# Performance work log

Measured on AMD Instinct MI355X. Metric: run time of the kernel, lower is better.

Reference implementation:

```python
import jax, jax.numpy as jnp
import numpy as np

SEQ = 2048
HIDDEN = 2048
INPUT = 2048
THETA = 3
TRUNC = 128  # truncated-BPTT length (divides SEQ)


def setup_inputs() -> dict:
    key = jax.random.key(0)
    k0, k1, k2, k3, k4 = jax.random.split(key, 5)
    inp = jax.random.normal(k0, (1, SEQ, INPUT), jnp.float32)
    internal = jax.random.normal(k1, (THETA + 1, SEQ, HIDDEN), jnp.float32) * 0.1
    state = jax.random.normal(k2, (1, 1, HIDDEN), jnp.float32) * 0.1
    weight_ih = jax.random.normal(k3, (HIDDEN, INPUT), jnp.float32) / np.sqrt(INPUT).astype(np.float32)
    weight_hh = jax.random.normal(k4, (HIDDEN, HIDDEN), jnp.float32) * np.float32(0.5 / np.sqrt(HIDDEN))
    bias = jnp.zeros((HIDDEN,), jnp.float32)
    return {"input": inp, "internal": internal, "state": state,
            "weight_ih": weight_ih, "weight_hh": weight_hh, "bias": bias,
            "theta": THETA}


def reference(input, internal, state, weight_ih, weight_hh, bias, theta):
    theta = int(theta)
    seq = input.shape[1]
    hidden = weight_hh.shape[0]
    # pad input along theta dim to theta+1 (torch: F.pad with zeros at the end of dim 0)
    x = jnp.pad(input, ((0, theta + 1 - input.shape[0]), (0, 0), (0, 0)))
    # Precompute the input-driven part of the cell for every (theta, t):
    # cell: h' = relu(x @ Wih^T + internal + bias + h @ Whh^T)
    pre = jnp.einsum('tsi,hi->tsh', x, weight_ih) + internal + bias  # [theta+1, seq, hidden]
    n_chunks = seq // TRUNC
    # [n_chunks, TRUNC, theta+1, hidden]
    pre_c = pre.transpose(1, 0, 2).reshape(n_chunks, TRUNC, theta + 1, hidden)

    def cell(p, h):
        return jax.nn.relu(p + h @ weight_hh.T)

    def step(h, pre_t):  # pre_t: [theta+1, hidden]
        h0 = cell(pre_t[0], h)
        outs = [h0]
        hth = h0
        for th in range(1, theta + 1):
            hth = cell(pre_t[th], hth)
            outs.append(hth)
        # continuousTheta=False: carry state from the base (th=0) step
        return h0, jnp.stack(outs, 0)  # [theta+1, hidden]

    def chunk(h, pre_chunk):
        h, outs = jax.lax.scan(step, h, pre_chunk)
        # truncated BPTT: detach state between chunks (identity in fwd)
        return jax.lax.stop_gradient(h), outs

    h0 = state[0, 0]  # [hidden]
    h_final, outs = jax.lax.scan(chunk, h0, pre_c)
    # outs: [n_chunks, TRUNC, theta+1, hidden] -> [theta+1, seq, hidden]
    outputs = outs.reshape(seq, theta + 1, hidden).transpose(1, 0, 2)
    return outputs, h_final[None, None, :]
```

## Files before the change

### kernel.cpp

```cpp
#include <hip/hip_runtime.h>
#include <stdint.h>

#define SEQ 2048
#define HID 2048
#define INP 2048
#define NTH 4
#define K3  (HID*3)

typedef uint32_t u32x4  __attribute__((ext_vector_type(4)));
typedef short    short8 __attribute__((ext_vector_type(8)));
typedef float    f32x4  __attribute__((ext_vector_type(4)));
typedef uint32_t uint4v __attribute__((ext_vector_type(4)));

template<int CTRL>
__device__ __forceinline__ float dpp_add(float x) {
    int y = __builtin_amdgcn_update_dpp(0, __float_as_int(x), CTRL, 0xF, 0xF, true);
    return x + __int_as_float(y);
}
__device__ __forceinline__ float wave_sum64(float x) {
    x = dpp_add<0x111>(x); x = dpp_add<0x112>(x); x = dpp_add<0x114>(x);
    x = dpp_add<0x118>(x); x = dpp_add<0x142>(x); x = dpp_add<0x143>(x);
    return x;
}

__device__ __forceinline__ ushort bf16h(float x) {
    uint32_t u = __float_as_uint(x);
    return (ushort)((u + 0x7fffu + ((u >> 16) & 1u)) >> 16);
}
template<int BSIDE>
__global__ __launch_bounds__(256)
void convert3_k(const float* __restrict__ X, ushort* __restrict__ X3) {
    const size_t t = (size_t)blockIdx.x * 256 + threadIdx.x;
    float xs[8];
    *reinterpret_cast<float4*>(&xs[0]) = *reinterpret_cast<const float4*>(X + t * 8);
    *reinterpret_cast<float4*>(&xs[4]) = *reinterpret_cast<const float4*>(X + t * 8 + 4);
    ushort o[24];
#pragma unroll
    for (int i = 0; i < 8; ++i) {
        const ushort hi = bf16h(xs[i]);
        const float hif = __uint_as_float(((uint32_t)hi) << 16);
        const ushort lo = bf16h(xs[i] - hif);
        o[i * 3 + 0] = hi;
        o[i * 3 + 1] = BSIDE ? lo : hi;
        o[i * 3 + 2] = BSIDE ? hi : lo;
    }
    ushort* pd = X3 + t * 24;
#pragma unroll
    for (int v = 0; v < 3; ++v)
        *reinterpret_cast<uint4v*>(pd + v * 8) = *reinterpret_cast<const uint4v*>(&o[v * 8]);
}

template<int RELU>
__global__ __launch_bounds__(256, 2)
void mfma_gemm(const ushort* __restrict__ A3, const ushort* __restrict__ B3,
               const float* __restrict__ D, const float* __restrict__ bias,
               float* __restrict__ C) {
    __shared__ ushort sA[128 * 64];
    __shared__ ushort sB[64 * 64];
    const int tid = threadIdx.x;
    const int w = tid >> 6, lane = tid & 63;
    const int m0 = blockIdx.y * 128, n0 = blockIdx.x * 64;

    f32x4 acc[2][4];
#pragma unroll
    for (int m = 0; m < 2; ++m)
#pragma unroll
        for (int n = 0; n < 4; ++n) acc[m][n] = (f32x4)0.f;

    const int c16s = (lane & 7) ^ ((lane >> 3) & 7);

    for (int kt = 0; kt < K3; kt += 64) {
#pragma unroll
        for (int i = 0; i < 4; ++i) {
            const int c = w * 4 + i;
            const int row = c * 8 + (lane >> 3);
            const ushort* src = A3 + (size_t)(m0 + row) * K3 + kt + c16s * 8;
            __builtin_amdgcn_global_load_lds(
                (const __attribute__((address_space(1))) uint32_t*)src,
                (__attribute__((address_space(3))) uint32_t*)(sA + c * 512), 16, 0, 0);
        }
#pragma unroll
        for (int i = 0; i < 2; ++i) {
            const int c = w * 2 + i;
            const int row = c * 8 + (lane >> 3);
            const ushort* src = B3 + (size_t)(n0 + row) * K3 + kt + c16s * 8;
            __builtin_amdgcn_global_load_lds(
                (const __attribute__((address_space(1))) uint32_t*)src,
                (__attribute__((address_space(3))) uint32_t*)(sB + c * 512), 16, 0, 0);
        }
        __syncthreads();

#pragma unroll
        for (int ks = 0; ks < 2; ++ks) {
            short8 af[2], bf[4];
#pragma unroll
            for (int m = 0; m < 2; ++m) {
                const int row = w * 32 + m * 16 + (lane & 15);
                const int c16 = (ks * 4 + (lane >> 4)) ^ (row & 7);
                af[m] = *reinterpret_cast<const short8*>(sA + row * 64 + c16 * 8);
            }
#pragma unroll
            for (int n = 0; n < 4; ++n) {
                const int row = n * 16 + (lane & 15);
                const int c16 = (ks * 4 + (lane >> 4)) ^ (row & 7);
                bf[n] = *reinterpret_cast<const short8*>(sB + row * 64 + c16 * 8);
            }
#pragma unroll
            for (int m = 0; m < 2; ++m)
#pragma unroll
                for (int n = 0; n < 4; ++n)
                    acc[m][n] = __builtin_amdgcn_mfma_f32_16x16x32_bf16(
                        af[m], bf[n], acc[m][n], 0, 0, 0);
        }
        __syncthreads();
    }

#pragma unroll
    for (int m = 0; m < 2; ++m)
#pragma unroll
        for (int n = 0; n < 4; ++n) {
            const int col = n0 + n * 16 + (lane & 15);
            const float bz = bias[col];
#pragma unroll
            for (int r = 0; r < 4; ++r) {
                const int rowm = m0 + w * 32 + m * 16 + (lane >> 4) * 4 + r;
                float v = acc[m][n][r] + D[(size_t)rowm * HID + col] + bz;
                if (RELU) v = fmaxf(v, 0.f);
                C[(size_t)rowm * HID + col] = v;
            }
        }
}

template<int RELU>
__global__ __launch_bounds__(256, 2)
void gemm_abt(const float* __restrict__ A, const float* __restrict__ B,
              const float* __restrict__ D, const float* __restrict__ bias,
              float* __restrict__ C, int M, int N, int K) {
    __shared__ float sA[16][132];
    __shared__ float sB[16][68];
    const int tid = threadIdx.x;
    const int tx = tid & 15, ty = tid >> 4;
    const int m0 = blockIdx.y * 128, n0 = blockIdx.x * 64;
    float acc[8][4];
#pragma unroll
    for (int i = 0; i < 8; ++i)
#pragma unroll
        for (int j = 0; j < 4; ++j) acc[i][j] = 0.f;
    const int srow = tid >> 2, skq = (tid & 3) * 4;
    for (int kt = 0; kt < K; kt += 16) {
#pragma unroll
        for (int s = 0; s < 2; ++s) {
            const int row = srow + s * 64;
            float4 va = *reinterpret_cast<const float4*>(&A[(size_t)(m0 + row) * K + kt + skq]);
            sA[skq + 0][row] = va.x; sA[skq + 1][row] = va.y;
            sA[skq + 2][row] = va.z; sA[skq + 3][row] = va.w;
        }
        {
            float4 vb = *reinterpret_cast<const float4*>(&B[(size_t)(n0 + srow) * K + kt + skq]);
            sB[skq + 0][srow] = vb.x; sB[skq + 1][srow] = vb.y;
            sB[skq + 2][srow] = vb.z; sB[skq + 3][srow] = vb.w;
        }
        __syncthreads();
#pragma unroll
        for (int k = 0; k < 16; ++k) {
            float a[8], b[4];
            *reinterpret_cast<float4*>(&a[0]) = *reinterpret_cast<const float4*>(&sA[k][ty * 8]);
            *reinterpret_cast<float4*>(&a[4]) = *reinterpret_cast<const float4*>(&sA[k][ty * 8 + 4]);
            *reinterpret_cast<float4*>(&b[0]) = *reinterpret_cast<const float4*>(&sB[k][tx * 4]);
#pragma unroll
            for (int i = 0; i < 8; ++i)
#pragma unroll
                for (int j = 0; j < 4; ++j) acc[i][j] = fmaf(a[i], b[j], acc[i][j]);
        }
        __syncthreads();
    }
#pragma unroll
    for (int i = 0; i < 8; ++i) {
        const size_t m = (size_t)(m0 + ty * 8 + i);
        const size_t n = (size_t)(n0 + tx * 4);
        float4 d = *reinterpret_cast<const float4*>(&D[m * N + n]);
        float4 bz = *reinterpret_cast<const float4*>(&bias[n]);
        float4 o;
        o.x = acc[i][0] + d.x + bz.x; o.y = acc[i][1] + d.y + bz.y;
        o.z = acc[i][2] + d.z + bz.z; o.w = acc[i][3] + d.w + bz.w;
        if (RELU) {
            o.x = fmaxf(o.x, 0.f); o.y = fmaxf(o.y, 0.f);
            o.z = fmaxf(o.z, 0.f); o.w = fmaxf(o.w, 0.f);
        }
        *reinterpret_cast<float4*>(&C[m * N + n]) = o;
    }
}

__global__ void init_state_k(const float* __restrict__ state,
                             unsigned long long* __restrict__ slots) {
    const int i = blockIdx.x * 256 + threadIdx.x;
    slots[i] = (unsigned long long)__float_as_uint(state[i]);
}

__global__ __launch_bounds__(1024, 1)
void rnn_scan(const float* __restrict__ Whh, float* __restrict__ out0,
              unsigned long long* __restrict__ slots, float* __restrict__ tail) {
    __shared__ float hl[HID];
    __shared__ float part[2][32];
    const int tid  = threadIdx.x;
    const int lane = tid & 63;
    const int wv   = tid >> 6;
    const int half = wv >> 3;
    const int g    = wv & 7;
    const int base = blockIdx.x * 32;
    const int kb   = half * 1024 + lane * 4;

    float4 wrow[4][4];
#pragma unroll
    for (int rr = 0; rr < 4; ++rr)
#pragma unroll
        for (int j = 0; j < 4; ++j)
            wrow[rr][j] = *reinterpret_cast<const float4*>(
                &Whh[(size_t)(base + g * 4 + rr) * HID + kb + j * 256]);

    for (int t = 0; t < SEQ; ++t) {
        float pre = 0.f;
        if (tid < 32) pre = out0[(size_t)t * HID + base + tid];

        const unsigned long long* sp =
            slots + (size_t)(t & 3) * HID + (size_t)tid * 2;
        const uint32_t tag = (uint32_t)t;
        u32x4 q;
        for (;;) {
            asm volatile(
                "global_load_dwordx4 %0, %1, off sc0 sc1\n\t"
                "s_waitcnt vmcnt(0)"
                : "=&v"(q) : "v"(sp) : "memory");
            if (q.y == tag && q.w == tag) break;
            __builtin_amdgcn_s_sleep(1);
        }
        hl[tid * 2 + 0] = __uint_as_float(q.x);
        hl[tid * 2 + 1] = __uint_as_float(q.z);
        __syncthreads();

        float acc0 = 0.f, acc1 = 0.f, acc2 = 0.f, acc3 = 0.f;
#pragma unroll
        for (int j = 0; j < 4; ++j) {
            const float4 hv = *reinterpret_cast<const float4*>(&hl[kb + j * 256]);
            acc0 = fmaf(wrow[0][j].x, hv.x, acc0); acc0 = fmaf(wrow[0][j].y, hv.y, acc0);
            acc0 = fmaf(wrow[0][j].z, hv.z, acc0); acc0 = fmaf(wrow[0][j].w, hv.w, acc0);
            acc1 = fmaf(wrow[1][j].x, hv.x, acc1); acc1 = fmaf(wrow[1][j].y, hv.y, acc1);
            acc1 = fmaf(wrow[1][j].z, hv.z, acc1); acc1 = fmaf(wrow[1][j].w, hv.w, acc1);
            acc2 = fmaf(wrow[2][j].x, hv.x, acc2); acc2 = fmaf(wrow[2][j].y, hv.y, acc2);
            acc2 = fmaf(wrow[2][j].z, hv.z, acc2); acc2 = fmaf(wrow[2][j].w, hv.w, acc2);
            acc3 = fmaf(wrow[3][j].x, hv.x, acc3); acc3 = fmaf(wrow[3][j].y, hv.y, acc3);
            acc3 = fmaf(wrow[3][j].z, hv.z, acc3); acc3 = fmaf(wrow[3][j].w, hv.w, acc3);
        }
        acc0 = wave_sum64(acc0); acc1 = wave_sum64(acc1);
        acc2 = wave_sum64(acc2); acc3 = wave_sum64(acc3);
        if (lane == 63)
            *reinterpret_cast<float4*>(&part[half][g * 4]) =
                make_float4(acc0, acc1, acc2, acc3);
        __syncthreads();

        if (tid < 32) {
            const int grow = base + tid;
            const float h = fmaxf(part[0][tid] + part[1][tid] + pre, 0.f);
            out0[(size_t)t * HID + grow] = h;
            const unsigned long long pk =
                ((unsigned long long)(uint32_t)(t + 1) << 32) | __float_as_uint(h);
            __hip_atomic_store(&slots[(size_t)((t + 1) & 3) * HID + grow], pk,
                               __ATOMIC_RELAXED, __HIP_MEMORY_SCOPE_AGENT);
            if (t == SEQ - 1) tail[grow] = h;
        }
    }
}

extern "C" void kernel_launch(void* const* d_in, const int* in_sizes, int n_in,
                              void* d_out, int out_size, void* d_ws, size_t ws_size,
                              hipStream_t stream) {
    const float* input    = (const float*)d_in[0];
    const float* internal = (const float*)d_in[1];
    const float* state    = (const float*)d_in[2];
    const float* wih      = (const float*)d_in[3];
    const float* whh      = (const float*)d_in[4];
    const float* bias     = (const float*)d_in[5];

    float* out = (float*)d_out;
    unsigned long long* slots = (unsigned long long*)d_ws;
    const size_t SH = (size_t)SEQ * HID;
    const size_t CVT = (size_t)HID * K3 * sizeof(ushort);
    const size_t need = 65536 + 3 * CVT;

    const dim3 cgrid((HID * INP / 8) / 256);
    if (ws_size >= need) {
        ushort* B3whh = (ushort*)((char*)d_ws + 65536);
        ushort* B3wih = (ushort*)((char*)d_ws + 65536 + CVT);
        ushort* A3    = (ushort*)((char*)d_ws + 65536 + 2 * CVT);

        convert3_k<1><<<cgrid, 256, 0, stream>>>(wih, B3wih);
        convert3_k<0><<<cgrid, 256, 0, stream>>>(input, A3);
        mfma_gemm<0><<<dim3(HID / 64, SEQ / 128), 256, 0, stream>>>(
            A3, B3wih, internal, bias, out);
        convert3_k<1><<<cgrid, 256, 0, stream>>>(whh, B3whh);
        init_state_k<<<8, 256, 0, stream>>>(state, slots);
        rnn_scan<<<64, 1024, 0, stream>>>(whh, out, slots, out + (size_t)NTH * SH);
        for (int th = 1; th < NTH; ++th) {
            convert3_k<0><<<cgrid, 256, 0, stream>>>(out + (size_t)(th - 1) * SH, A3);
            mfma_gemm<1><<<dim3(HID / 64, SEQ / 128), 256, 0, stream>>>(
                A3, B3whh, internal + (size_t)th * SH, bias, out + (size_t)th * SH);
        }
    } else {
        gemm_abt<0><<<dim3(HID / 64, SEQ / 128), 256, 0, stream>>>(
            input, wih, internal, bias, out, SEQ, HID, INP);
        init_state_k<<<8, 256, 0, stream>>>(state, slots);
        rnn_scan<<<64, 1024, 0, stream>>>(whh, out, slots, out + (size_t)NTH * SH);
        for (int th = 1; th < NTH; ++th)
            gemm_abt<1><<<dim3(HID / 64, SEQ / 128), 256, 0, stream>>>(
                out + (size_t)(th - 1) * SH, whh, internal + (size_t)th * SH, bias,
                out + (size_t)th * SH, SEQ, HID, HID);
    }
}
```

Measured before the change: 3.884 ms.

## Restructure recurrent scan to 512 threads, full-row waves, one barrier per step

```diff
diff --git a/kernel.cpp b/kernel.cpp
--- a/kernel.cpp
+++ b/kernel.cpp
@@ -131,117 +131,58 @@
         }
 }
 
-template<int RELU>
-__global__ __launch_bounds__(256, 2)
-void gemm_abt(const float* __restrict__ A, const float* __restrict__ B,
-              const float* __restrict__ D, const float* __restrict__ bias,
-              float* __restrict__ C, int M, int N, int K) {
-    __shared__ float sA[16][132];
-    __shared__ float sB[16][68];
-    const int tid = threadIdx.x;
-    const int tx = tid & 15, ty = tid >> 4;
-    const int m0 = blockIdx.y * 128, n0 = blockIdx.x * 64;
-    float acc[8][4];
-#pragma unroll
-    for (int i = 0; i < 8; ++i)
-#pragma unroll
-        for (int j = 0; j < 4; ++j) acc[i][j] = 0.f;
-    const int srow = tid >> 2, skq = (tid & 3) * 4;
-    for (int kt = 0; kt < K; kt += 16) {
-#pragma unroll
-        for (int s = 0; s < 2; ++s) {
-            const int row = srow + s * 64;
-            float4 va = *reinterpret_cast<const float4*>(&A[(size_t)(m0 + row) * K + kt + skq]);
-            sA[skq + 0][row] = va.x; sA[skq + 1][row] = va.y;
-            sA[skq + 2][row] = va.z; sA[skq + 3][row] = va.w;
-        }
-        {
-            float4 vb = *reinterpret_cast<const float4*>(&B[(size_t)(n0 + srow) * K + kt + skq]);
-            sB[skq + 0][srow] = vb.x; sB[skq + 1][srow] = vb.y;
-            sB[skq + 2][srow] = vb.z; sB[skq + 3][srow] = vb.w;
-        }
-        __syncthreads();
-#pragma unroll
-        for (int k = 0; k < 16; ++k) {
-            float a[8], b[4];
-            *reinterpret_cast<float4*>(&a[0]) = *reinterpret_cast<const float4*>(&sA[k][ty * 8]);
-            *reinterpret_cast<float4*>(&a[4]) = *reinterpret_cast<const float4*>(&sA[k][ty * 8 + 4]);
-            *reinterpret_cast<float4*>(&b[0]) = *reinterpret_cast<const float4*>(&sB[k][tx * 4]);
-#pragma unroll
-            for (int i = 0; i < 8; ++i)
-#pragma unroll
-                for (int j = 0; j < 4; ++j) acc[i][j] = fmaf(a[i], b[j], acc[i][j]);
-        }
-        __syncthreads();
-    }
-#pragma unroll
-    for (int i = 0; i < 8; ++i) {
-        const size_t m = (size_t)(m0 + ty * 8 + i);
-        const size_t n = (size_t)(n0 + tx * 4);
-        float4 d = *reinterpret_cast<const float4*>(&D[m * N + n]);
-        float4 bz = *reinterpret_cast<const float4*>(&bias[n]);
-        float4 o;
-        o.x = acc[i][0] + d.x + bz.x; o.y = acc[i][1] + d.y + bz.y;
-        o.z = acc[i][2] + d.z + bz.z; o.w = acc[i][3] + d.w + bz.w;
-        if (RELU) {
-            o.x = fmaxf(o.x, 0.f); o.y = fmaxf(o.y, 0.f);
-            o.z = fmaxf(o.z, 0.f); o.w = fmaxf(o.w, 0.f);
-        }
-        *reinterpret_cast<float4*>(&C[m * N + n]) = o;
-    }
-}
-
 __global__ void init_state_k(const float* __restrict__ state,
                              unsigned long long* __restrict__ slots) {
     const int i = blockIdx.x * 256 + threadIdx.x;
     slots[i] = (unsigned long long)__float_as_uint(state[i]);
 }
 
-__global__ __launch_bounds__(1024, 1)
+__global__ __launch_bounds__(512, 1)
 void rnn_scan(const float* __restrict__ Whh, float* __restrict__ out0,
               unsigned long long* __restrict__ slots, float* __restrict__ tail) {
-    __shared__ float hl[HID];
-    __shared__ float part[2][32];
+    __shared__ float hl[2][HID];
     const int tid  = threadIdx.x;
     const int lane = tid & 63;
-    const int wv   = tid >> 6;
-    const int half = wv >> 3;
-    const int g    = wv & 7;
+    const int w    = tid >> 6;
     const int base = blockIdx.x * 32;
-    const int kb   = half * 1024 + lane * 4;
-
-    float4 wrow[4][4];
+    const int kb   = lane * 4;
+
+    float4 wrow[4][8];
 #pragma unroll
     for (int rr = 0; rr < 4; ++rr)
 #pragma unroll
-        for (int j = 0; j < 4; ++j)
+        for (int j = 0; j < 8; ++j)
             wrow[rr][j] = *reinterpret_cast<const float4*>(
-                &Whh[(size_t)(base + g * 4 + rr) * HID + kb + j * 256]);
+                &Whh[(size_t)(base + 4 * w + rr) * HID + kb + j * 256]);
 
     for (int t = 0; t < SEQ; ++t) {
-        float pre = 0.f;
-        if (tid < 32) pre = out0[(size_t)t * HID + base + tid];
+        float4 pre4 = make_float4(0.f, 0.f, 0.f, 0.f);
+        if (lane == 63)
+            pre4 = *reinterpret_cast<const float4*>(&out0[(size_t)t * HID + base + 4 * w]);
 
         const unsigned long long* sp =
-            slots + (size_t)(t & 3) * HID + (size_t)tid * 2;
+            slots + (size_t)(t & 3) * HID + (size_t)tid * 4;
         const uint32_t tag = (uint32_t)t;
-        u32x4 q;
+        u32x4 q0, q1;
         for (;;) {
             asm volatile(
-                "global_load_dwordx4 %0, %1, off sc0 sc1\n\t"
+                "global_load_dwordx4 %0, %2, off sc0 sc1\n\t"
+                "global_load_dwordx4 %1, %2, off offset:16 sc0 sc1\n\t"
                 "s_waitcnt vmcnt(0)"
-                : "=&v"(q) : "v"(sp) : "memory");
-            if (q.y == tag && q.w == tag) break;
+                : "=&v"(q0), "=&v"(q1) : "v"(sp) : "memory");
+            if (q0.y == tag && q0.w == tag && q1.y == tag && q1.w == tag) break;
             __builtin_amdgcn_s_sleep(1);
         }
-        hl[tid * 2 + 0] = __uint_as_float(q.x);
-        hl[tid * 2 + 1] = __uint_as_float(q.z);
+        *reinterpret_cast<float4*>(&hl[t & 1][tid * 4]) =
+            make_float4(__uint_as_float(q0.x), __uint_as_float(q0.z),
+                        __uint_as_float(q1.x), __uint_as_float(q1.z));
         __syncthreads();
 
+        const float* hb = hl[t & 1];
         float acc0 = 0.f, acc1 = 0.f, acc2 = 0.f, acc3 = 0.f;
 #pragma unroll
-        for (int j = 0; j < 4; ++j) {
-            const float4 hv = *reinterpret_cast<const float4*>(&hl[kb + j * 256]);
+        for (int j = 0; j < 8; ++j) {
+            const float4 hv = *reinterpret_cast<const float4*>(&hb[kb + j * 256]);
             acc0 = fmaf(wrow[0][j].x, hv.x, acc0); acc0 = fmaf(wrow[0][j].y, hv.y, acc0);
             acc0 = fmaf(wrow[0][j].z, hv.z, acc0); acc0 = fmaf(wrow[0][j].w, hv.w, acc0);
             acc1 = fmaf(wrow[1][j].x, hv.x, acc1); acc1 = fmaf(wrow[1][j].y, hv.y, acc1);
@@ -253,20 +194,27 @@
         }
         acc0 = wave_sum64(acc0); acc1 = wave_sum64(acc1);
         acc2 = wave_sum64(acc2); acc3 = wave_sum64(acc3);
-        if (lane == 63)
-            *reinterpret_cast<float4*>(&part[half][g * 4]) =
-                make_float4(acc0, acc1, acc2, acc3);
-        __syncthreads();
-
-        if (tid < 32) {
-            const int grow = base + tid;
-            const float h = fmaxf(part[0][tid] + part[1][tid] + pre, 0.f);
-            out0[(size_t)t * HID + grow] = h;
-            const unsigned long long pk =
-                ((unsigned long long)(uint32_t)(t + 1) << 32) | __float_as_uint(h);
-            __hip_atomic_store(&slots[(size_t)((t + 1) & 3) * HID + grow], pk,
-                               __ATOMIC_RELAXED, __HIP_MEMORY_SCOPE_AGENT);
-            if (t == SEQ - 1) tail[grow] = h;
+
+        if (lane == 63) {
+            const float h0 = fmaxf(acc0 + pre4.x, 0.f);
+            const float h1 = fmaxf(acc1 + pre4.y, 0.f);
+            const float h2 = fmaxf(acc2 + pre4.z, 0.f);
+            const float h3 = fmaxf(acc3 + pre4.w, 0.f);
+            const int grow = base + 4 * w;
+            *reinterpret_cast<float4*>(&out0[(size_t)t * HID + grow]) =
+                make_float4(h0, h1, h2, h3);
+            unsigned long long* ps = slots + (size_t)((t + 1) & 3) * HID + grow;
+            const unsigned long long tg = (unsigned long long)(uint32_t)(t + 1) << 32;
+            __hip_atomic_store(ps + 0, tg | __float_as_uint(h0),
+                               __ATOMIC_RELAXED, __HIP_MEMORY_SCOPE_AGENT);
+            __hip_atomic_store(ps + 1, tg | __float_as_uint(h1),
+                               __ATOMIC_RELAXED, __HIP_MEMORY_SCOPE_AGENT);
+            __hip_atomic_store(ps + 2, tg | __float_as_uint(h2),
+                               __ATOMIC_RELAXED, __HIP_MEMORY_SCOPE_AGENT);
+            __hip_atomic_store(ps + 3, tg | __float_as_uint(h3),
+                               __ATOMIC_RELAXED, __HIP_MEMORY_SCOPE_AGENT);
+            if (t == SEQ - 1)
+                *reinterpret_cast<float4*>(&tail[grow]) = make_float4(h0, h1, h2, h3);
         }
     }
 }
@@ -299,20 +247,14 @@
             A3, B3wih, internal, bias, out);
         convert3_k<1><<<cgrid, 256, 0, stream>>>(whh, B3whh);
         init_state_k<<<8, 256, 0, stream>>>(state, slots);
-        rnn_scan<<<64, 1024, 0, stream>>>(whh, out, slots, out + (size_t)NTH * SH);
+        rnn_scan<<<64, 512, 0, stream>>>(whh, out, slots, out + (size_t)NTH * SH);
         for (int th = 1; th < NTH; ++th) {
             convert3_k<0><<<cgrid, 256, 0, stream>>>(out + (size_t)(th - 1) * SH, A3);
             mfma_gemm<1><<<dim3(HID / 64, SEQ / 128), 256, 0, stream>>>(
                 A3, B3whh, internal + (size_t)th * SH, bias, out + (size_t)th * SH);
         }
     } else {
-        gemm_abt<0><<<dim3(HID / 64, SEQ / 128), 256, 0, stream>>>(
-            input, wih, internal, bias, out, SEQ, HID, INP);
         init_state_k<<<8, 256, 0, stream>>>(state, slots);
-        rnn_scan<<<64, 1024, 0, stream>>>(whh, out, slots, out + (size_t)NTH * SH);
-        for (int th = 1; th < NTH; ++th)
-            gemm_abt<1><<<dim3(HID / 64, SEQ / 128), 256, 0, stream>>>(
-                out + (size_t)(th - 1) * SH, whh, internal + (size_t)th * SH, bias,
-                out + (size_t)th * SH, SEQ, HID, HID);
-    }
-}
+        rnn_scan<<<64, 512, 0, stream>>>(whh, out, slots, out + (size_t)NTH * SH);
+    }
+}
```

New measurement: 8.199 ms. +111.1%, slower.
